# Performance work log

Measured on AMD Instinct MI355X. Metric: run time of the kernel, lower is better.

Reference implementation:

```python
import jax, jax.numpy as jnp
import numpy as np

N_EMBED = 8192
BETA = 0.25


def setup_inputs() -> dict:
    key = jax.random.key(0)
    k1, k2 = jax.random.split(key)
    z = jax.random.normal(k1, (16, 256, 32, 32), dtype=jnp.float32)
    # matches nn.Embedding init uniform_(-1/n_embed, 1/n_embed)
    embed_weight = jax.random.uniform(k2, (N_EMBED, 256), dtype=jnp.float32,
                                      minval=-1.0 / N_EMBED, maxval=1.0 / N_EMBED)
    return {"z": z, "embed_weight": embed_weight}


def reference(z, embed_weight):
    sg = jax.lax.stop_gradient
    # b c h w -> b h w c
    z_nhwc = jnp.transpose(z, (0, 2, 3, 1))
    # squared L2 distance to every code: ||z||^2 + ||e||^2 - 2 z.e  -> [b,h,w,n]
    d = (jnp.sum(z_nhwc ** 2, axis=-1, keepdims=True)
         + jnp.sum(embed_weight ** 2, axis=1)
         - 2.0 * jnp.einsum('bhwc,nc->bhwn', z_nhwc, embed_weight))
    indices = jnp.argmin(d, axis=-1)            # [b,h,w] int
    z_q = embed_weight[indices]                  # [b,h,w,c] gather

    loss = (BETA * jnp.mean((sg(z_q) - z_nhwc) ** 2)
            + jnp.mean((z_q - sg(z_nhwc)) ** 2))

    # straight-through estimator
    z_q_st = z_nhwc + sg(z_q - z_nhwc)
    out = jnp.transpose(z_q_st, (0, 3, 1, 2))    # b h w c -> b c h w

    # perplexity via histogram (equivalent to one_hot(...).mean(0))
    flat = indices.reshape(-1)
    counts = jnp.zeros((N_EMBED,), dtype=jnp.float32).at[flat].add(1.0)
    avg_probs = counts / flat.shape[0]
    perplexity = jnp.exp(-jnp.sum(avg_probs * jnp.log(avg_probs + 1e-10)))

    return (out, indices, loss, perplexity)
```

## Files before the change

### kernel.cpp

```cpp
#include <hip/hip_runtime.h>
#include <stdint.h>

typedef unsigned long long u64;
typedef unsigned int u32;

#define CDIM 256
#define NCODES 8192
#define MTOT 16384
#define OUT_ELEMS 4194304
#define BETA 0.25f

#define WS_PACKED 0u
#define WS_ENORM  131072u
#define WS_ZSQ    163840u
#define WS_COUNTS 229376u
#define WS_LOSS   262144u
#define WS_ZB     524544u
#define WS_EB     8913152u
#define WS_TT2    13107456u
#define WS_NEEDED 21496064u

typedef short bf16x8 __attribute__((ext_vector_type(8)));
typedef float f32x4 __attribute__((ext_vector_type(4)));

#define GL2LDS16(g, l) __builtin_amdgcn_global_load_lds(            \
    (const __attribute__((address_space(1))) void*)(g),             \
    (__attribute__((address_space(3))) void*)(l), 16, 0, 0)

__device__ __forceinline__ unsigned short f2bf(float f) {
  u32 u = __float_as_uint(f);
  u32 r = (u + 0x7FFFu + ((u >> 16) & 1u)) >> 16;
  return (unsigned short)r;
}

__global__ void conv_kernel(const float* __restrict__ z, const float* __restrict__ E,
                            unsigned short* __restrict__ zb, unsigned short* __restrict__ eb,
                            float* __restrict__ zsq, float* __restrict__ enorm) {
  int blk = blockIdx.x;
  int t = threadIdx.x, w = t >> 6, lane = t & 63;
  if (blk < 256) {
    __shared__ unsigned short tz[64][66];
    __shared__ float part[4][4][64];
    int b = blk >> 4, p0 = (blk & 15) << 6;
    const float* zp = z + ((size_t)b << 18) + p0;
    #pragma unroll
    for (int ct = 0; ct < 4; ++ct) {
      int c0 = ct << 6;
      if (ct) __syncthreads();
      float s = 0.f;
      #pragma unroll
      for (int i = 0; i < 16; ++i) {
        int cl = w + (i << 2);
        float v = zp[((size_t)(c0 + cl) << 10) + lane];
        s = fmaf(v, v, s);
        tz[cl][lane] = f2bf(v);
      }
      part[ct][w][lane] = s;
      __syncthreads();
      #pragma unroll
      for (int j = 0; j < 16; ++j) {
        int pl = w + (j << 2);
        zb[(((size_t)b << 10) + p0 + pl) * 256 + c0 + lane] = tz[lane][pl];
      }
    }
    if (w == 0) {
      float q0 = ((part[0][0][lane] + part[0][1][lane]) + part[0][2][lane]) + part[0][3][lane];
      float q1 = ((part[1][0][lane] + part[1][1][lane]) + part[1][2][lane]) + part[1][3][lane];
      float q2 = ((part[2][0][lane] + part[2][1][lane]) + part[2][2][lane]) + part[2][3][lane];
      float q3 = ((part[3][0][lane] + part[3][1][lane]) + part[3][2][lane]) + part[3][3][lane];
      zsq[(b << 10) + p0 + lane] = ((q0 + q1) + q2) + q3;
    }
  } else {
    int e4 = blk - 256;
    size_t base = ((size_t)e4 << 11) + ((size_t)t << 3);
    float4 v0 = *(const float4*)&E[base];
    float4 v1 = *(const float4*)&E[base + 4];
    ushort4 o0 = { f2bf(v0.x), f2bf(v0.y), f2bf(v0.z), f2bf(v0.w) };
    ushort4 o1 = { f2bf(v1.x), f2bf(v1.y), f2bf(v1.z), f2bf(v1.w) };
    *(ushort4*)&eb[base] = o0;
    *(ushort4*)&eb[base + 4] = o1;
    float s = v0.x * v0.x + v0.y * v0.y + v0.z * v0.z + v0.w * v0.w
            + v1.x * v1.x + v1.y * v1.y + v1.z * v1.z + v1.w * v1.w;
    #pragma unroll
    for (int off = 16; off; off >>= 1) s += __shfl_xor(s, off, 32);
    if ((t & 31) == 0) enorm[(e4 << 3) + (t >> 5)] = s;
  }
}

__global__ __launch_bounds__(512, 1) void gemm_kernel(
    const unsigned short* __restrict__ zb, const unsigned short* __restrict__ eb,
    uint2* __restrict__ tt2) {
  __shared__ unsigned short As[2][256 * 64];
  __shared__ unsigned short Bs[2][256 * 64];
  const int t = threadIdx.x;
  const int w = t >> 6, lane = t & 63;
  const int wm = w >> 1, wn = w & 1;
  const int r16 = lane & 15, kg = lane >> 4, r7 = r16 & 7;
  const int m0 = blockIdx.x << 8, n0 = blockIdx.y << 8;

  f32x4 acc[4][8];
  #pragma unroll
  for (int i = 0; i < 4; ++i)
    #pragma unroll
    for (int j = 0; j < 8; ++j) acc[i][j] = (f32x4)0.f;

  const int jsw = ((t & 7) ^ ((t >> 3) & 7)) << 3;
  const unsigned short* zsrc = zb + (((size_t)m0 + (t >> 3)) << 8) + jsw;
  const unsigned short* esrc = eb + (((size_t)n0 + (t >> 3)) << 8) + jsw;

  const int abase = ((wm << 6) + r16) << 7;
  const int bbase = ((wn << 7) + r16) << 7;
  const int jx0 = (kg ^ r7) << 4;
  const int jx1 = ((4 + kg) ^ r7) << 4;

  #pragma unroll
  for (int i = 0; i < 4; ++i) {
    GL2LDS16(zsrc + (i << 14), (char*)As[0] + (i << 13) + (t << 4));
    GL2LDS16(esrc + (i << 14), (char*)Bs[0] + (i << 13) + (t << 4));
  }
  __syncthreads();

  #pragma unroll
  for (int kt = 0; kt < 4; ++kt) {
    const int cur = kt & 1;
    if (kt < 3) {
      const int ko = (kt + 1) << 6;
      #pragma unroll
      for (int i = 0; i < 4; ++i) {
        GL2LDS16(zsrc + (i << 14) + ko, (char*)As[cur ^ 1] + (i << 13) + (t << 4));
        GL2LDS16(esrc + (i << 14) + ko, (char*)Bs[cur ^ 1] + (i << 13) + (t << 4));
      }
    }
    #pragma unroll
    for (int s = 0; s < 2; ++s) {
      const int jx = s ? jx1 : jx0;
      bf16x8 af[4], bq[8];
      #pragma unroll
      for (int mi = 0; mi < 4; ++mi)
        af[mi] = *(const bf16x8*)((const char*)As[cur] + abase + (mi << 11) + jx);
      #pragma unroll
      for (int ni = 0; ni < 8; ++ni)
        bq[ni] = *(const bf16x8*)((const char*)Bs[cur] + bbase + (ni << 11) + jx);
      __builtin_amdgcn_s_setprio(1);
      #pragma unroll
      for (int mi = 0; mi < 4; ++mi)
        #pragma unroll
        for (int ni = 0; ni < 8; ++ni)
          acc[mi][ni] = __builtin_amdgcn_mfma_f32_16x16x32_bf16(bq[ni], af[mi], acc[mi][ni], 0, 0, 0);
      __builtin_amdgcn_s_setprio(0);
    }
    __syncthreads();
  }

  const u32 kgr = (u32)(kg << 2);
  #pragma unroll
  for (int mi = 0; mi < 4; ++mi) {
    float a1 = 0.f, a2 = 0.f;
    #pragma unroll
    for (int ni = 0; ni < 8; ++ni) {
      #pragma unroll
      for (int reg = 0; reg < 4; ++reg) {
        u32 e = __float_as_uint(acc[mi][ni][reg] + 2.0f);
        float k = __uint_as_float((e & 0xFFFFFF80u) | ((u32)(ni << 4) | kgr | (u32)reg));
        float na2 = __builtin_amdgcn_fmed3f(a1, a2, k);
        a1 = fmaxf(a1, k);
        a2 = na2;
      }
    }
    #pragma unroll
    for (int off = 16; off < 64; off <<= 1) {
      float b1 = __shfl_xor(a1, off, 64);
      float b2 = __shfl_xor(a2, off, 64);
      a2 = fmaxf(fminf(a1, b1), fmaxf(a2, b2));
      a1 = fmaxf(a1, b1);
    }
    if (kg == 0) {
      int row = m0 + (wm << 6) + (mi << 4) + r16;
      int tile = (blockIdx.y << 1) + wn;
      tt2[((size_t)tile << 14) + row] =
          make_uint2(__float_as_uint(a1), __float_as_uint(a2));
    }
  }
}

__global__ __launch_bounds__(256) void refine_kernel(
    const float* __restrict__ z, const float* __restrict__ E,
    const float* __restrict__ zsq, const float* __restrict__ enorm,
    const uint2* __restrict__ tt2, u64* __restrict__ packed,
    float* __restrict__ out_idx, u32* __restrict__ counts) {
  __shared__ uint2 tc[64][33];
  __shared__ float zrow[32][260];
  const int t = threadIdx.x, w = t >> 6, lane = t & 63;
  const int m0 = blockIdx.x << 5;
  const int b = m0 >> 10, p0 = m0 & 1023;

  #pragma unroll
  for (int i = 0; i < 8; ++i) {
    int tau = (i << 3) + (t >> 5);
    tc[tau][t & 31] = tt2[((size_t)tau << 14) + m0 + (t & 31)];
  }
  #pragma unroll
  for (int i = 0; i < 8; ++i) {
    int c = (i << 5) + (t >> 3);
    int p4 = (t & 7) << 2;
    float4 v = *(const float4*)&z[((size_t)b << 18) + ((size_t)c << 10) + p0 + p4];
    zrow[p4 + 0][c] = v.x;
    zrow[p4 + 1][c] = v.y;
    zrow[p4 + 2][c] = v.z;
    zrow[p4 + 3][c] = v.w;
  }
  __syncthreads();

  for (int j = 0; j < 8; ++j) {
    const int rr = (w << 3) + j;
    const int m = m0 + rr;
    uint2 c = tc[lane][rr];
    float f0 = __uint_as_float(c.x), f1 = __uint_as_float(c.y);
    float fm = f0;
    #pragma unroll
    for (int off = 1; off < 64; off <<= 1) fm = fmaxf(fm, __shfl_xor(fm, off, 64));
    float thr = fm - 1.5e-4f;
    const float4 zr4 = *(const float4*)&zrow[rr][lane << 2];
    float zsqm = zsq[m];
    u64 best = ~0ull;
    #pragma unroll
    for (int s = 0; s < 2; ++s) {
      u32 ck = s ? c.y : c.x;
      float fv = s ? f1 : f0;
      u64 mask = __ballot(fv >= thr);
      while (mask) {
        int src = __ffsll((unsigned long long)mask) - 1;
        mask &= mask - 1;
        u32 key = (u32)__shfl((int)ck, src, 64);
        int idx = (src << 7) | (int)(key & 127u);
        const float4 e4 = *(const float4*)&E[(size_t)idx * CDIM + (lane << 2)];
        float pa = zr4.x * e4.x;
        pa = fmaf(zr4.y, e4.y, pa);
        pa = fmaf(zr4.z, e4.z, pa);
        pa = fmaf(zr4.w, e4.w, pa);
        #pragma unroll
        for (int off = 1; off < 64; off <<= 1) pa += __shfl_xor(pa, off, 64);
        float ttv = zsqm + enorm[idx];
        float d = ttv - 2.0f * pa;
        u64 k2 = ((u64)__float_as_uint(d) << 32) | (u32)idx;
        if (k2 < best) best = k2;
      }
    }
    if (lane == 0) {
      packed[m] = best;
      int idx = (int)(u32)(best & 0xffffffffull);
      out_idx[m] = (float)idx;
      atomicAdd(&counts[idx], 1u);
    }
  }
}

__global__ void enorm_kernel(const float* __restrict__ E, float* __restrict__ enorm) {
  int wave = threadIdx.x >> 6;
  int lane = threadIdx.x & 63;
  int n = blockIdx.x * 4 + wave;
  float4 v = reinterpret_cast<const float4*>(E + (size_t)n * CDIM)[lane];
  float s = v.x * v.x + v.y * v.y + v.z * v.z + v.w * v.w;
  #pragma unroll
  for (int off = 32; off; off >>= 1) s += __shfl_down(s, off, 64);
  if (lane == 0) enorm[n] = s;
}

__global__ void zsq_kernel(const float* __restrict__ z, float* __restrict__ zsq) {
  int blk = blockIdx.x;
  int j = threadIdx.x;
  int b = blk >> 2;
  int p = ((blk & 3) << 8) + j;
  const float* zp = z + (size_t)b * (CDIM * 1024) + p;
  float acc = 0.f;
  #pragma unroll 8
  for (int c = 0; c < CDIM; ++c) {
    float v = zp[(size_t)c * 1024];
    acc += v * v;
  }
  zsq[(blk << 8) + j] = acc;
}

#define BM 128
#define BN 128
#define BK 32
__global__ __launch_bounds__(256, 2) void dist_kernel(
    const float* __restrict__ z, const float* __restrict__ E,
    const float* __restrict__ zsq, const float* __restrict__ enorm,
    unsigned long long* __restrict__ packed) {
  __shared__ float zs[BK][BM];
  __shared__ float es[BK][BN];
  const int t = threadIdx.x;
  const int m0 = blockIdx.x * BM;
  const int n0 = blockIdx.y * BN;
  const int b = m0 >> 10;
  const int p0 = m0 & 1023;
  const int zc = t >> 5;
  const int zm = (t & 31) << 2;
  const float* zbase = z + (size_t)b * 262144 + p0 + zm;
  const int en = t & 127;
  const int ec = (t >> 7) << 4;
  const float* ebase = E + (size_t)(n0 + en) * CDIM + ec;
  float4 zr[4], er[4];
  #pragma unroll
  for (int r = 0; r < 4; ++r)
    zr[r] = *(const float4*)(zbase + (size_t)(r * 8 + zc) * 1024);
  #pragma unroll
  for (int i = 0; i < 4; ++i)
    er[i] = *(const float4*)(ebase + 4 * i);
  float acc[8][8];
  #pragma unroll
  for (int a = 0; a < 8; ++a)
    #pragma unroll
    for (int bb = 0; bb < 8; ++bb) acc[a][bb] = 0.f;
  const int tx = t & 15, ty = t >> 4;
  for (int kt = 0; kt < CDIM / BK; ++kt) {
    __syncthreads();
    #pragma unroll
    for (int r = 0; r < 4; ++r)
      *(float4*)&zs[r * 8 + zc][zm] = zr[r];
    #pragma unroll
    for (int i = 0; i < 4; ++i) {
      es[ec + 4 * i + 0][en] = er[i].x;
      es[ec + 4 * i + 1][en] = er[i].y;
      es[ec + 4 * i + 2][en] = er[i].z;
      es[ec + 4 * i + 3][en] = er[i].w;
    }
    __syncthreads();
    if (kt + 1 < CDIM / BK) {
      const int c0 = (kt + 1) * BK;
      #pragma unroll
      for (int r = 0; r < 4; ++r)
        zr[r] = *(const float4*)(zbase + (size_t)(c0 + r * 8 + zc) * 1024);
      #pragma unroll
      for (int i = 0; i < 4; ++i)
        er[i] = *(const float4*)(ebase + c0 + 4 * i);
    }
    #pragma unroll 8
    for (int kk = 0; kk < BK; ++kk) {
      float4 za = *(const float4*)&zs[kk][ty * 4];
      float4 zb4 = *(const float4*)&zs[kk][64 + ty * 4];
      float4 ea = *(const float4*)&es[kk][tx * 4];
      float4 eb4 = *(const float4*)&es[kk][64 + tx * 4];
      float zv[8] = {za.x, za.y, za.z, za.w, zb4.x, zb4.y, zb4.z, zb4.w};
      float ev[8] = {ea.x, ea.y, ea.z, ea.w, eb4.x, eb4.y, eb4.z, eb4.w};
      #pragma unroll
      for (int a = 0; a < 8; ++a)
        #pragma unroll
        for (int bb = 0; bb < 8; ++bb)
          acc[a][bb] += zv[a] * ev[bb];
    }
  }
  #pragma unroll
  for (int a = 0; a < 8; ++a) {
    int rloc = (a < 4) ? (ty * 4 + a) : (64 + ty * 4 + (a - 4));
    float zq = zsq[m0 + rloc];
    float bestd = 3.4e38f;
    int bestn = 0;
    #pragma unroll
    for (int bb = 0; bb < 8; ++bb) {
      int nloc = (bb < 4) ? (tx * 4 + bb) : (64 + tx * 4 + (bb - 4));
      int n = n0 + nloc;
      float ttv = zq + enorm[n];
      float d = ttv - 2.0f * acc[a][bb];
      if (d < bestd) { bestd = d; bestn = n; }
    }
    unsigned long long pk =
        ((unsigned long long)__float_as_uint(bestd) << 32) | (unsigned)bestn;
    #pragma unroll
    for (int off = 1; off < 16; off <<= 1) {
      unsigned long long other = __shfl_xor(pk, off, 16);
      if (other < pk) pk = other;
    }
    if (tx == 0) atomicMin(&packed[m0 + rloc], pk);
  }
}

__global__ void idx_kernel(const unsigned long long* __restrict__ packed,
                           float* __restrict__ out_idx, unsigned int* __restrict__ counts) {
  int m = blockIdx.x * 256 + threadIdx.x;
  int idx = (int)(unsigned)(packed[m] & 0xffffffffull);
  out_idx[m] = (float)idx;
  atomicAdd(&counts[idx], 1u);
}

__global__ __launch_bounds__(256) void out_kernel(
    const float* __restrict__ z, const float* __restrict__ E,
    const u64* __restrict__ packed,
    float* __restrict__ out, float* __restrict__ loss_acc) {
  __shared__ float es[32][257];
  const int t = threadIdx.x, w = t >> 6, lane = t & 63;
  const int m0 = blockIdx.x << 5;
  const int b = m0 >> 10, p0 = m0 & 1023;

  #pragma unroll
  for (int i = 0; i < 8; ++i) {
    int pl = (w << 3) + i;
    int idx = (int)(u32)(packed[m0 + pl] & 0xffffffffull);
    float4 v = *(const float4*)&E[((size_t)idx << 8) + (lane << 2)];
    es[pl][(lane << 2) + 0] = v.x;
    es[pl][(lane << 2) + 1] = v.y;
    es[pl][(lane << 2) + 2] = v.z;
    es[pl][(lane << 2) + 3] = v.w;
  }
  __syncthreads();

  const int pp = lane & 31, chi = lane >> 5;
  const size_t gbase = ((size_t)b << 18) + p0 + pp;
  float s = 0.f;
  #pragma unroll 8
  for (int i = 0; i < 32; ++i) {
    int c = (i << 3) + (w << 1) + chi;
    float zv = z[gbase + ((size_t)c << 10)];
    float e = es[pp][c];
    float diff = e - zv;
    out[gbase + ((size_t)c << 10)] = zv + diff;
    s = fmaf(diff, diff, s);
  }
  #pragma unroll
  for (int off = 32; off; off >>= 1) s += __shfl_down(s, off, 64);
  __shared__ float red[4];
  if (lane == 0) red[w] = s;
  __syncthreads();
  if (t == 0) atomicAdd(loss_acc, red[0] + red[1] + red[2] + red[3]);
}

__global__ void scalar_kernel(const unsigned int* __restrict__ counts,
                              const float* __restrict__ loss_acc,
                              float* __restrict__ out) {
  float s = 0.f;
  for (int i = threadIdx.x; i < NCODES; i += 256) {
    float pl = (float)counts[i] * (1.0f / 16384.0f);
    s += pl * logf(pl + 1e-10f);
  }
  #pragma unroll
  for (int off = 32; off; off >>= 1) s += __shfl_down(s, off, 64);
  __shared__ float red[4];
  int wv = threadIdx.x >> 6, lane = threadIdx.x & 63;
  if (lane == 0) red[wv] = s;
  __syncthreads();
  if (threadIdx.x == 0) {
    float tot = red[0] + red[1] + red[2] + red[3];
    out[OUT_ELEMS + MTOT] = (1.0f + BETA) * loss_acc[0] * (1.0f / (float)OUT_ELEMS);
    out[OUT_ELEMS + MTOT + 1] = expf(-tot);
  }
}

extern "C" void kernel_launch(void* const* d_in, const int* in_sizes, int n_in,
                              void* d_out, int out_size, void* d_ws, size_t ws_size,
                              hipStream_t stream) {
  const float* z = (const float*)d_in[0];
  const float* E = (const float*)d_in[1];
  float* out = (float*)d_out;
  char* ws = (char*)d_ws;
  u64* packed = (u64*)(ws + WS_PACKED);
  float* enorm = (float*)(ws + WS_ENORM);
  float* zsq = (float*)(ws + WS_ZSQ);
  u32* counts = (u32*)(ws + WS_COUNTS);
  float* loss_acc = (float*)(ws + WS_LOSS);

  hipMemsetAsync(counts, 0, 32768 + 256, stream);

  if (ws_size >= WS_NEEDED) {
    unsigned short* zb = (unsigned short*)(ws + WS_ZB);
    unsigned short* ebuf = (unsigned short*)(ws + WS_EB);
    uint2* tt2 = (uint2*)(ws + WS_TT2);
    conv_kernel<<<1280, 256, 0, stream>>>(z, E, zb, ebuf, zsq, enorm);
    dim3 g(MTOT / 256, NCODES / 256);
    gemm_kernel<<<g, 512, 0, stream>>>(zb, ebuf, tt2);
    refine_kernel<<<MTOT / 32, 256, 0, stream>>>(z, E, zsq, enorm, tt2, packed,
                                                 out + OUT_ELEMS, counts);
  } else {
    hipMemsetAsync(packed, 0xFF, MTOT * 8, stream);
    enorm_kernel<<<NCODES / 4, 256, 0, stream>>>(E, enorm);
    zsq_kernel<<<64, 256, 0, stream>>>(z, zsq);
    dim3 g(MTOT / BM, NCODES / BN);
    dist_kernel<<<g, 256, 0, stream>>>(z, E, zsq, enorm, packed);
    idx_kernel<<<MTOT / 256, 256, 0, stream>>>(packed, out + OUT_ELEMS, counts);
  }

  out_kernel<<<MTOT / 32, 256, 0, stream>>>(z, E, packed, out, loss_acc);
  scalar_kernel<<<1, 256, 0, stream>>>(counts, loss_acc, out);
}
```

Measured before the change: 138.2 us.

## Fuse output/loss into refine kernel, swizzle GEMM blocks, and finer-grain GEMM pipelining

The refine kernel now keeps the winning codebook row in registers, writes the straight-through output and accumulates the commitment loss itself, so the separate out_kernel pass (re-gather E and re-read z) is skipped on the main path. The GEMM remaps block indices into a grouped order for better L2 reuse of z/E tiles. It also splits each k-substep into two halves with global-to-LDS prefetch interleaved between MFMA groups and explicit waitcnt/barrier sync. This adds more barriers per iteration and relies on the hand-placed waitcnts being correct.

```diff
diff --git a/kernel.cpp b/kernel.cpp
--- a/kernel.cpp
+++ b/kernel.cpp
@@ -96,7 +96,12 @@
   const int w = t >> 6, lane = t & 63;
   const int wm = w >> 1, wn = w & 1;
   const int r16 = lane & 15, kg = lane >> 4, r7 = r16 & 7;
-  const int m0 = blockIdx.x << 8, n0 = blockIdx.y << 8;
+
+  const int lin = ((int)blockIdx.y << 6) + (int)blockIdx.x;
+  const int xk = lin & 7, loc = lin >> 3;
+  const int bx = ((xk & 3) << 4) | (loc & 15);
+  const int by = ((xk >> 2) << 4) | (loc >> 4);
+  const int m0 = bx << 8, n0 = by << 8;
 
   f32x4 acc[4][8];
   #pragma unroll
@@ -110,46 +115,67 @@
 
   const int abase = ((wm << 6) + r16) << 7;
   const int bbase = ((wn << 7) + r16) << 7;
-  const int jx0 = (kg ^ r7) << 4;
-  const int jx1 = ((4 + kg) ^ r7) << 4;
 
   #pragma unroll
   for (int i = 0; i < 4; ++i) {
     GL2LDS16(zsrc + (i << 14), (char*)As[0] + (i << 13) + (t << 4));
     GL2LDS16(esrc + (i << 14), (char*)Bs[0] + (i << 13) + (t << 4));
   }
-  __syncthreads();
 
   #pragma unroll
   for (int kt = 0; kt < 4; ++kt) {
     const int cur = kt & 1;
-    if (kt < 3) {
-      const int ko = (kt + 1) << 6;
-      #pragma unroll
-      for (int i = 0; i < 4; ++i) {
-        GL2LDS16(zsrc + (i << 14) + ko, (char*)As[cur ^ 1] + (i << 13) + (t << 4));
-        GL2LDS16(esrc + (i << 14) + ko, (char*)Bs[cur ^ 1] + (i << 13) + (t << 4));
+    const char* Ab = (const char*)As[cur];
+    const char* Bb = (const char*)Bs[cur];
+    char* An = (char*)As[cur ^ 1];
+    char* Bn = (char*)Bs[cur ^ 1];
+    const int ko = (kt + 1) << 6;
+    asm volatile("s_waitcnt vmcnt(0)" ::: "memory");
+    __builtin_amdgcn_s_barrier();
+    #pragma unroll
+    for (int s = 0; s < 2; ++s) {
+      const int jx = (((s << 2) | kg) ^ r7) << 4;
+      bf16x8 af[4], bq[4], bq2[4];
+      #pragma unroll
+      for (int mi = 0; mi < 4; ++mi)
+        af[mi] = *(const bf16x8*)(Ab + abase + (mi << 11) + jx);
+      #pragma unroll
+      for (int ni = 0; ni < 4; ++ni)
+        bq[ni] = *(const bf16x8*)(Bb + bbase + (ni << 11) + jx);
+      if (kt < 3) {
+        const int p = s << 1;
+        GL2LDS16(zsrc + (p << 14) + ko, An + (p << 13) + (t << 4));
+        GL2LDS16(esrc + (p << 14) + ko, Bn + (p << 13) + (t << 4));
       }
-    }
-    #pragma unroll
-    for (int s = 0; s < 2; ++s) {
-      const int jx = s ? jx1 : jx0;
-      bf16x8 af[4], bq[8];
-      #pragma unroll
-      for (int mi = 0; mi < 4; ++mi)
-        af[mi] = *(const bf16x8*)((const char*)As[cur] + abase + (mi << 11) + jx);
-      #pragma unroll
-      for (int ni = 0; ni < 8; ++ni)
-        bq[ni] = *(const bf16x8*)((const char*)Bs[cur] + bbase + (ni << 11) + jx);
+      asm volatile("s_waitcnt lgkmcnt(0)" ::: "memory");
+      __builtin_amdgcn_s_barrier();
       __builtin_amdgcn_s_setprio(1);
       #pragma unroll
       for (int mi = 0; mi < 4; ++mi)
         #pragma unroll
-        for (int ni = 0; ni < 8; ++ni)
+        for (int ni = 0; ni < 4; ++ni)
           acc[mi][ni] = __builtin_amdgcn_mfma_f32_16x16x32_bf16(bq[ni], af[mi], acc[mi][ni], 0, 0, 0);
       __builtin_amdgcn_s_setprio(0);
-    }
-    __syncthreads();
+      __builtin_amdgcn_s_barrier();
+      #pragma unroll
+      for (int ni = 0; ni < 4; ++ni)
+        bq2[ni] = *(const bf16x8*)(Bb + bbase + ((4 + ni) << 11) + jx);
+      if (kt < 3) {
+        const int p = (s << 1) | 1;
+        GL2LDS16(zsrc + (p << 14) + ko, An + (p << 13) + (t << 4));
+        GL2LDS16(esrc + (p << 14) + ko, Bn + (p << 13) + (t << 4));
+      }
+      asm volatile("s_waitcnt lgkmcnt(0)" ::: "memory");
+      __builtin_amdgcn_s_barrier();
+      __builtin_amdgcn_s_setprio(1);
+      #pragma unroll
+      for (int mi = 0; mi < 4; ++mi)
+        #pragma unroll
+        for (int ni = 0; ni < 4; ++ni)
+          acc[mi][4 + ni] = __builtin_amdgcn_mfma_f32_16x16x32_bf16(bq2[ni], af[mi], acc[mi][4 + ni], 0, 0, 0);
+      __builtin_amdgcn_s_setprio(0);
+      __builtin_amdgcn_s_barrier();
+    }
   }
 
   const u32 kgr = (u32)(kg << 2);
@@ -176,20 +202,22 @@
     }
     if (kg == 0) {
       int row = m0 + (wm << 6) + (mi << 4) + r16;
-      int tile = (blockIdx.y << 1) + wn;
+      int tile = (by << 1) + wn;
       tt2[((size_t)tile << 14) + row] =
           make_uint2(__float_as_uint(a1), __float_as_uint(a2));
     }
   }
 }
 
-__global__ __launch_bounds__(256) void refine_kernel(
+__global__ __launch_bounds__(256) void refine_out_kernel(
     const float* __restrict__ z, const float* __restrict__ E,
     const float* __restrict__ zsq, const float* __restrict__ enorm,
     const uint2* __restrict__ tt2, u64* __restrict__ packed,
-    float* __restrict__ out_idx, u32* __restrict__ counts) {
+    float* __restrict__ out, float* __restrict__ out_idx,
+    u32* __restrict__ counts, float* __restrict__ loss_acc) {
   __shared__ uint2 tc[64][33];
   __shared__ float zrow[32][260];
+  __shared__ float red[4];
   const int t = threadIdx.x, w = t >> 6, lane = t & 63;
   const int m0 = blockIdx.x << 5;
   const int b = m0 >> 10, p0 = m0 & 1023;
@@ -211,6 +239,7 @@
   }
   __syncthreads();
 
+  float wloss = 0.f;
   for (int j = 0; j < 8; ++j) {
     const int rr = (w << 3) + j;
     const int m = m0 + rr;
@@ -223,6 +252,7 @@
     const float4 zr4 = *(const float4*)&zrow[rr][lane << 2];
     float zsqm = zsq[m];
     u64 best = ~0ull;
+    float4 be4 = {0.f, 0.f, 0.f, 0.f};
     #pragma unroll
     for (int s = 0; s < 2; ++s) {
       u32 ck = s ? c.y : c.x;
@@ -243,15 +273,38 @@
         float ttv = zsqm + enorm[idx];
         float d = ttv - 2.0f * pa;
         u64 k2 = ((u64)__float_as_uint(d) << 32) | (u32)idx;
-        if (k2 < best) best = k2;
+        bool better = k2 < best;
+        best = better ? k2 : best;
+        be4 = better ? e4 : be4;
       }
     }
+    float4 df, o4;
+    df.x = be4.x - zr4.x; df.y = be4.y - zr4.y; df.z = be4.z - zr4.z; df.w = be4.w - zr4.w;
+    o4.x = zr4.x + df.x;  o4.y = zr4.y + df.y;  o4.z = zr4.z + df.z;  o4.w = zr4.w + df.w;
+    wloss = fmaf(df.x, df.x, wloss);
+    wloss = fmaf(df.y, df.y, wloss);
+    wloss = fmaf(df.z, df.z, wloss);
+    wloss = fmaf(df.w, df.w, wloss);
+    *(float4*)&zrow[rr][lane << 2] = o4;
     if (lane == 0) {
       packed[m] = best;
       int idx = (int)(u32)(best & 0xffffffffull);
       out_idx[m] = (float)idx;
       atomicAdd(&counts[idx], 1u);
     }
+  }
+  #pragma unroll
+  for (int off = 32; off; off >>= 1) wloss += __shfl_down(wloss, off, 64);
+  if (lane == 0) red[w] = wloss;
+  __syncthreads();
+  if (t == 0) atomicAdd(loss_acc, red[0] + red[1] + red[2] + red[3]);
+
+  #pragma unroll
+  for (int i = 0; i < 8; ++i) {
+    int c = (i << 5) + (t >> 3);
+    int p4 = (t & 7) << 2;
+    float4 o = { zrow[p4 + 0][c], zrow[p4 + 1][c], zrow[p4 + 2][c], zrow[p4 + 3][c] };
+    *(float4*)&out[((size_t)b << 18) + ((size_t)c << 10) + p0 + p4] = o;
   }
 }
 
@@ -392,7 +445,6 @@
   const int t = threadIdx.x, w = t >> 6, lane = t & 63;
   const int m0 = blockIdx.x << 5;
   const int b = m0 >> 10, p0 = m0 & 1023;
-
   #pragma unroll
   for (int i = 0; i < 8; ++i) {
     int pl = (w << 3) + i;
@@ -404,7 +456,6 @@
     es[pl][(lane << 2) + 3] = v.w;
   }
   __syncthreads();
-
   const int pp = lane & 31, chi = lane >> 5;
   const size_t gbase = ((size_t)b << 18) + p0 + pp;
   float s = 0.f;
@@ -468,8 +519,8 @@
     conv_kernel<<<1280, 256, 0, stream>>>(z, E, zb, ebuf, zsq, enorm);
     dim3 g(MTOT / 256, NCODES / 256);
     gemm_kernel<<<g, 512, 0, stream>>>(zb, ebuf, tt2);
-    refine_kernel<<<MTOT / 32, 256, 0, stream>>>(z, E, zsq, enorm, tt2, packed,
-                                                 out + OUT_ELEMS, counts);
+    refine_out_kernel<<<MTOT / 32, 256, 0, stream>>>(z, E, zsq, enorm, tt2, packed,
+                                                     out, out + OUT_ELEMS, counts, loss_acc);
   } else {
     hipMemsetAsync(packed, 0xFF, MTOT * 8, stream);
     enorm_kernel<<<NCODES / 4, 256, 0, stream>>>(E, enorm);
@@ -477,8 +528,8 @@
     dim3 g(MTOT / BM, NCODES / BN);
     dist_kernel<<<g, 256, 0, stream>>>(z, E, zsq, enorm, packed);
     idx_kernel<<<MTOT / 256, 256, 0, stream>>>(packed, out + OUT_ELEMS, counts);
-  }
-
-  out_kernel<<<MTOT / 32, 256, 0, stream>>>(z, E, packed, out, loss_acc);
+    out_kernel<<<MTOT / 32, 256, 0, stream>>>(z, E, packed, out, loss_acc);
+  }
+
   scalar_kernel<<<1, 256, 0, stream>>>(counts, loss_acc, out);
 }
```

Result: slower. 156.2 us (+13.0%).
